# Kernel tuning notes

Hardware: AMD Instinct MI355X
Metric: run time of the kernel (lower is better)

The kernel has to match this reference:

```python
import jax, jax.numpy as jnp
import numpy as np

N_CH = 64
EPS = 1e-5


def _lhat():
    # adj=None branch: dist = ones - eye; adj_dist = exp(-dist/std) (torch.std is unbiased).
    dist = np.ones((N_CH, N_CH), np.float32) - np.eye(N_CH, dtype=np.float32)
    std = dist.std(ddof=1)
    A = np.exp(-dist / std).astype(np.float32)  # all entries > threshold=1e-4 -> fully connected w/ self loops
    deg = A.sum(axis=1)
    dinv = 1.0 / np.sqrt(deg)
    L = np.eye(N_CH, dtype=np.float32) - dinv[:, None] * A * dinv[None, :]  # sym-normalized Laplacian
    # ChebConv rescaling: Lhat = 2L/lambda_max - I with lambda_max=2 -> L - I
    return jnp.asarray(L - np.eye(N_CH, dtype=np.float32))


def _cheb(x, Lhat, W):
    # x: (B, N, Fin), W: (K, Fin, Fout). Chebyshev recursion, bias=False.
    Tx0 = x
    out = jnp.einsum('bnf,fo->bno', Tx0, W[0])
    Tx1 = jnp.einsum('nm,bmf->bnf', Lhat, Tx0)
    out = out + jnp.einsum('bnf,fo->bno', Tx1, W[1])
    for k in range(2, W.shape[0]):
        Tx2 = 2.0 * jnp.einsum('nm,bmf->bnf', Lhat, Tx1) - Tx0
        out = out + jnp.einsum('bnf,fo->bno', Tx2, W[k])
        Tx0, Tx1 = Tx1, Tx2
    return out


def _bn(x, g, b):
    # PyG BatchNorm (training mode): stats over all nodes in the batch -> axes (0,1).
    mu = jnp.mean(x, axis=(0, 1), keepdims=True)
    var = jnp.mean((x - mu) ** 2, axis=(0, 1), keepdims=True)
    return g * (x - mu) * jax.lax.rsqrt(var + EPS) + b


def setup_inputs() -> dict:
    key = jax.random.key(0)
    ks = jax.random.split(key, 4)
    B, F_IN, D = 4096, 256, 128
    x = jax.random.normal(ks[0], (B, N_CH, F_IN), dtype=jnp.float32)
    W1 = jax.random.normal(ks[1], (5, F_IN, D), dtype=jnp.float32) * 0.05
    W2 = jax.random.normal(ks[2], (3, D, D), dtype=jnp.float32) * 0.08
    W3 = jax.random.normal(ks[3], (3, D, D), dtype=jnp.float32) * 0.08
    ones = jnp.ones((D,), jnp.float32)
    zeros = jnp.zeros((D,), jnp.float32)
    return {'x': x, 'W1': W1, 'W2': W2, 'W3': W3,
            'g1': ones, 'b1': zeros, 'g2': ones, 'b2': zeros, 'g3': ones, 'b3': zeros}


def reference(x, W1, W2, W3, g1, b1, g2, b2, g3, b3):
    Lhat = _lhat()
    h = jax.nn.relu(_bn(_cheb(x, Lhat, W1), g1, b1))
    h = jax.nn.relu(_bn(_cheb(h, Lhat, W2), g2, b2))
    h = jax.nn.relu(_bn(_cheb(h, Lhat, W3), g3, b3))
    # global_mean_pool over nodes of each graph (dropout p=0 is identity)
    return jnp.mean(h, axis=1)  # (B, embed_dim)
```

## Files before the change

kernel.cpp:

```cpp
#include <hip/hip_runtime.h>
#include <cmath>


typedef __attribute__((ext_vector_type(8))) short bf16x8;
typedef __attribute__((ext_vector_type(4))) float f32x4;

typedef __attribute__((address_space(1))) const unsigned int guint_t;
typedef __attribute__((address_space(3))) unsigned int luint_t;

constexpr int BATCH = 4096;
constexpr int DCH   = 128;
constexpr float INV_NROWS = 1.0f / 262144.0f;

constexpr size_t OFF_G1   = 0;
constexpr size_t OFF_G2   = 32768;
constexpr size_t OFF_G3   = 49152;
constexpr size_t OFF_SCSH = 65536;
constexpr size_t OFF_PP   = 66304;
constexpr size_t OFF_Y    = 1180416;

struct Coeffs { float a[5]; float b[5]; };

__device__ __forceinline__ unsigned short f2bf(float f) {
  unsigned u = __float_as_uint(f);
  u += 0x7FFFu + ((u >> 16) & 1u);
  return (unsigned short)(u >> 16);
}
__device__ __forceinline__ float bf2f(unsigned short s) {
  return __uint_as_float(((unsigned)s) << 16);
}

__global__ __launch_bounds__(256) void prep_gran(const float* __restrict__ W1,
                                                 const float* __restrict__ W2,
                                                 const float* __restrict__ W3,
                                                 float* __restrict__ ws, Coeffs co)
{
  int id = blockIdx.x * 256 + threadIdx.x;
  const float* W; int CIN, K, r; const float* cf; unsigned short* dst;
  if (id < 8192) {
    W = W1; CIN = 256; K = 5; r = id & 4095;
    cf = (id >= 4096) ? co.b : co.a;
    dst = (unsigned short*)(ws + OFF_G1) + (size_t)id * 8;
  } else if (id < 12288) {
    int e = id - 8192; W = W2; CIN = 128; K = 3; r = e & 2047;
    cf = (e >= 2048) ? co.b : co.a;
    dst = (unsigned short*)(ws + OFF_G2) + (size_t)e * 8;
  } else {
    int e = id - 12288; W = W3; CIN = 128; K = 3; r = e & 2047;
    cf = (e >= 2048) ? co.b : co.a;
    dst = (unsigned short*)(ws + OFF_G3) + (size_t)e * 8;
  }
  int kt  = r >> 9;
  int ct  = (r >> 6) & 7;
  int ln  = r & 63;
  int col = ct * 16 + (ln & 15);
  int f0  = kt * 32 + (ln >> 4) * 8;
  bf16x8 g;
#pragma unroll
  for (int i = 0; i < 8; ++i) {
    float s = 0.f;
    for (int k = 0; k < K; ++k)
      s = fmaf(cf[k], W[((size_t)k * CIN + f0 + i) * DCH + col], s);
    g[i] = (short)f2bf(s);
  }
  *reinterpret_cast<bf16x8*>(dst) = g;
}

template <int CIN, bool FIRST>
__global__ __launch_bounds__(512) void layer_k(
    const float* __restrict__ inF,
    const unsigned short* __restrict__ inB,
    unsigned short* __restrict__ yout,
    const unsigned short* __restrict__ gran,
    const float* __restrict__ scsh,
    float* __restrict__ part)
{
  constexpr int NKT = CIN / 32;
  constexpr int NG  = CIN * 16;

  __shared__ unsigned short sB[CIN * 256];
  __shared__ unsigned short slab[8][1152];
  __shared__ float sJw[4][2][DCH];
  __shared__ float sScale[DCH];
  __shared__ float sShift[DCH];

  const int tid = threadIdx.x;
  const int wv  = tid >> 6;
  const int p   = wv >> 1;
  const int h   = wv & 1;
  const int l   = tid & 63;
  const int lr  = l & 15;
  const int lk  = l >> 4;

  {
    const char* gB = reinterpret_cast<const char*>(gran);
    char* lB = reinterpret_cast<char*>(&sB[0]);
#pragma unroll
    for (int i = 0; i < (CIN * 512) / 8192; ++i) {
      const int c = i * 8 + wv;
      __builtin_amdgcn_global_load_lds(
          (guint_t*)(gB + (size_t)c * 1024 + (size_t)l * 16),
          (luint_t*)(lB + c * 1024), 16, 0, 0);
    }
  }
  if constexpr (!FIRST) {
    if (tid < DCH) {
      sScale[tid] = scsh[tid];
      sShift[tid] = scsh[DCH + tid];
    }
  }
  __syncthreads();

  const bf16x8* sBu = reinterpret_cast<const bf16x8*>(&sB[0]);

  float psum[8], psq[8];
#pragma unroll
  for (int ct = 0; ct < 8; ++ct) { psum[ct] = 0.f; psq[ct] = 0.f; }

#pragma unroll 1
  for (int it = 0; it < 4; ++it) {
    const int batch = blockIdx.x * 16 + it * 4 + p;

    f32x4 acc[8][2];
    f32x4 accJ[8];
#pragma unroll
    for (int ct = 0; ct < 8; ++ct) {
#pragma unroll
      for (int mt = 0; mt < 2; ++mt)
#pragma unroll
        for (int r = 0; r < 4; ++r) acc[ct][mt][r] = 0.f;
#pragma unroll
      for (int r = 0; r < 4; ++r) accJ[ct][r] = 0.f;
    }

#pragma unroll
    for (int kt = 0; kt < NKT; ++kt) {
      bf16x8 af[2];
      float vs[8];
#pragma unroll
      for (int i = 0; i < 8; ++i) vs[i] = 0.f;

      if constexpr (FIRST) {
        const float* ap = inF + ((size_t)batch * 64 + h * 32 + lr) * CIN + kt * 32 + lk * 8;
#pragma unroll
        for (int mt = 0; mt < 2; ++mt) {
          float4 u0 = *reinterpret_cast<const float4*>(ap + (size_t)mt * 16 * CIN);
          float4 u1 = *reinterpret_cast<const float4*>(ap + (size_t)mt * 16 * CIN + 4);
          float v8[8] = {u0.x, u0.y, u0.z, u0.w, u1.x, u1.y, u1.z, u1.w};
#pragma unroll
          for (int i = 0; i < 8; ++i) {
            vs[i] += v8[i];
            af[mt][i] = (short)f2bf(v8[i]);
          }
        }
      } else {
        const int c0 = kt * 32 + lk * 8;
        const float4 s0 = *reinterpret_cast<const float4*>(&sScale[c0]);
        const float4 s1 = *reinterpret_cast<const float4*>(&sScale[c0 + 4]);
        const float4 h0 = *reinterpret_cast<const float4*>(&sShift[c0]);
        const float4 h1 = *reinterpret_cast<const float4*>(&sShift[c0 + 4]);
        const float scv[8] = {s0.x, s0.y, s0.z, s0.w, s1.x, s1.y, s1.z, s1.w};
        const float shv[8] = {h0.x, h0.y, h0.z, h0.w, h1.x, h1.y, h1.z, h1.w};
        const bf16x8* yb = reinterpret_cast<const bf16x8*>(inB + (size_t)batch * 8192);
#pragma unroll
        for (int mt = 0; mt < 2; ++mt) {
          bf16x8 r16 = yb[kt * 256 + (h * 2 + mt) * 64 + l];
#pragma unroll
          for (int i = 0; i < 8; ++i) {
            float hv = fmaxf(fmaf(bf2f((unsigned short)r16[i]), scv[i], shv[i]), 0.f);
            vs[i] += hv;
            af[mt][i] = (short)f2bf(hv);
          }
        }
      }

      bf16x8 asum;
#pragma unroll
      for (int i = 0; i < 8; ++i) asum[i] = (short)f2bf(vs[i]);

      const bf16x8* bI = sBu + kt * 512 + l;
#pragma unroll
      for (int ct = 0; ct < 8; ++ct) {
        bf16x8 fI = bI[ct * 64];
        acc[ct][0] = __builtin_amdgcn_mfma_f32_16x16x32_bf16(af[0], fI, acc[ct][0], 0, 0, 0);
        acc[ct][1] = __builtin_amdgcn_mfma_f32_16x16x32_bf16(af[1], fI, acc[ct][1], 0, 0, 0);
      }
      const bf16x8* bJ = bI + NG;
#pragma unroll
      for (int ct = 0; ct < 8; ++ct)
        accJ[ct] = __builtin_amdgcn_mfma_f32_16x16x32_bf16(asum, bJ[ct * 64], accJ[ct], 0, 0, 0);
    }

#pragma unroll
    for (int ct = 0; ct < 8; ++ct) {
      float t = (accJ[ct][0] + accJ[ct][1]) + (accJ[ct][2] + accJ[ct][3]);
      t += __shfl_xor(t, 16);
      t += __shfl_xor(t, 32);
      if (lk == 0) sJw[p][h][ct * 16 + lr] = t;
    }
    __syncthreads();
    float jv[8];
#pragma unroll
    for (int ct = 0; ct < 8; ++ct)
      jv[ct] = sJw[p][0][ct * 16 + lr] + sJw[p][1][ct * 16 + lr];
    __syncthreads();

    unsigned short* myT = &slab[wv][0];
    bf16x8* yo = reinterpret_cast<bf16x8*>(yout + (size_t)batch * 8192);
#pragma unroll
    for (int mt = 0; mt < 2; ++mt) {
      const int m = h * 2 + mt;
#pragma unroll
      for (int cp = 0; cp < 2; ++cp) {
#pragma unroll
        for (int cq = 0; cq < 4; ++cq) {
          const int ct = cp * 4 + cq;
#pragma unroll
          for (int r = 0; r < 4; ++r) {
            float val = acc[ct][mt][r] + jv[ct];
            psum[ct] += val;
            psq[ct]  = fmaf(val, val, psq[ct]);
            myT[(lk * 4 + r) * 72 + cq * 16 + lr] = f2bf(val);
          }
        }
#pragma unroll
        for (int k2 = 0; k2 < 2; ++k2) {
          bf16x8 gd = *reinterpret_cast<const bf16x8*>(&myT[lr * 72 + k2 * 32 + lk * 8]);
          yo[(cp * 2 + k2) * 256 + m * 64 + l] = gd;
        }
      }
    }
  }

#pragma unroll
  for (int ct = 0; ct < 8; ++ct) {
    psum[ct] += __shfl_xor(psum[ct], 16);
    psum[ct] += __shfl_xor(psum[ct], 32);
    psq[ct]  += __shfl_xor(psq[ct], 16);
    psq[ct]  += __shfl_xor(psq[ct], 32);
  }
  if (lk == 0) {
    float* sRedW = reinterpret_cast<float*>(&slab[wv][0]);
#pragma unroll
    for (int ct = 0; ct < 8; ++ct) {
      sRedW[ct * 16 + lr]       = psum[ct];
      sRedW[128 + ct * 16 + lr] = psq[ct];
    }
  }
  __syncthreads();
  if (tid < 256) {
    const float* base = reinterpret_cast<const float*>(&slab[0][0]);
    float tot = 0.f;
#pragma unroll
    for (int w2 = 0; w2 < 8; ++w2) tot += base[w2 * 576 + tid];
    part[(size_t)blockIdx.x * 256 + tid] = tot;
  }
}

__global__ __launch_bounds__(1024) void finB_k(const float* __restrict__ pp,
                                               const float* __restrict__ gam,
                                               const float* __restrict__ bet,
                                               float* __restrict__ scsh)
{
  __shared__ float red[4][256];
  __shared__ float tot[256];
  const int q = threadIdx.x >> 8, t = threadIdx.x & 255;
  float s = 0.f;
#pragma unroll 8
  for (int i = 0; i < 64; ++i)
    s += pp[(size_t)(q * 64 + i) * 256 + t];
  red[q][t] = s;
  __syncthreads();
  if (q == 0) tot[t] = (red[0][t] + red[1][t]) + (red[2][t] + red[3][t]);
  __syncthreads();
  if (threadIdx.x < 128) {
    float mu  = tot[threadIdx.x] * INV_NROWS;
    float var = tot[128 + threadIdx.x] * INV_NROWS - mu * mu;
    float rs  = rsqrtf(var + 1e-5f);
    float sc  = gam[threadIdx.x] * rs;
    scsh[threadIdx.x]       = sc;
    scsh[128 + threadIdx.x] = fmaf(-mu, sc, bet[threadIdx.x]);
  }
}

__global__ __launch_bounds__(256) void pool_k(const unsigned short* __restrict__ y,
                                              const float* __restrict__ scsh,
                                              float* __restrict__ out)
{
  __shared__ float sYp[64][132];
  __shared__ float sPool[2][DCH];
  const int b = blockIdx.x;
  const int t = threadIdx.x;
  const int wv = t >> 6, l = t & 63;
  const int row = wv * 16 + (l & 15);

#pragma unroll
  for (int kt = 0; kt < 4; ++kt) {
    bf16x8 r16 = *(reinterpret_cast<const bf16x8*>(y + (size_t)b * 8192) + (kt * 256 + t));
    const int feat = kt * 32 + (l >> 4) * 8;
    float4 f0, f1;
    f0.x = bf2f((unsigned short)r16[0]); f0.y = bf2f((unsigned short)r16[1]);
    f0.z = bf2f((unsigned short)r16[2]); f0.w = bf2f((unsigned short)r16[3]);
    f1.x = bf2f((unsigned short)r16[4]); f1.y = bf2f((unsigned short)r16[5]);
    f1.z = bf2f((unsigned short)r16[6]); f1.w = bf2f((unsigned short)r16[7]);
    *reinterpret_cast<float4*>(&sYp[row][feat])     = f0;
    *reinterpret_cast<float4*>(&sYp[row][feat + 4]) = f1;
  }
  __syncthreads();
  {
    const int c = t & 127, rg = t >> 7;
    float sc = scsh[c];
    float sh = scsh[128 + c];
    float s = 0.f;
#pragma unroll 8
    for (int r = rg * 32; r < rg * 32 + 32; ++r)
      s += fmaxf(fmaf(sYp[r][c], sc, sh), 0.f);
    sPool[rg][c] = s;
  }
  __syncthreads();
  if (t < DCH)
    out[(size_t)b * DCH + t] = (sPool[0][t] + sPool[1][t]) * (1.0f / 64.0f);
}

extern "C" void kernel_launch(void* const* d_in, const int* in_sizes, int n_in,
                              void* d_out, int out_size, void* d_ws, size_t ws_size,
                              hipStream_t stream)
{
  const float* x  = (const float*)d_in[0];
  const float* W1 = (const float*)d_in[1];
  const float* W2 = (const float*)d_in[2];
  const float* W3 = (const float*)d_in[3];
  const float* g1 = (const float*)d_in[4];
  const float* b1 = (const float*)d_in[5];
  const float* g2 = (const float*)d_in[6];
  const float* b2 = (const float*)d_in[7];
  const float* g3 = (const float*)d_in[8];
  const float* b3 = (const float*)d_in[9];
  float* out = (float*)d_out;
  float* ws  = (float*)d_ws;

  Coeffs co;
  {
    double sd  = sqrt(63.0 / 4095.0);
    double av  = exp(-1.0 / sd);
    double deg = 1.0 + 63.0 * av;
    double al  = -(1.0 - av) / deg;
    double be  = -av / deg;
    double ak[5], bk[5];
    ak[0] = 1.0; bk[0] = 0.0;
    ak[1] = al;  bk[1] = be;
    for (int k = 2; k < 5; ++k) {
      ak[k] = 2.0 * al * ak[k - 1] - ak[k - 2];
      bk[k] = 2.0 * (be * ak[k - 1] + (al + 64.0 * be) * bk[k - 1]) - bk[k - 2];
    }
    for (int k = 0; k < 5; ++k) { co.a[k] = (float)ak[k]; co.b[k] = (float)bk[k]; }
  }

  const unsigned short* gr1 = (const unsigned short*)(ws + OFF_G1);
  const unsigned short* gr2 = (const unsigned short*)(ws + OFF_G2);
  const unsigned short* gr3 = (const unsigned short*)(ws + OFF_G3);
  float* scsh1 = ws + OFF_SCSH;
  float* scsh2 = scsh1 + 256;
  float* scsh3 = scsh1 + 512;
  float* pp    = ws + OFF_PP;
  unsigned short* yv = (unsigned short*)(ws + OFF_Y);

  prep_gran<<<64, 256, 0, stream>>>(W1, W2, W3, ws, co);

  layer_k<256, true ><<<256, 512, 0, stream>>>(x, nullptr, yv, gr1, nullptr, pp);
  finB_k<<<1, 1024, 0, stream>>>(pp, g1, b1, scsh1);
  layer_k<128, false><<<256, 512, 0, stream>>>(nullptr, yv, yv, gr2, scsh1, pp);
  finB_k<<<1, 1024, 0, stream>>>(pp, g2, b2, scsh2);
  layer_k<128, false><<<256, 512, 0, stream>>>(nullptr, yv, yv, gr3, scsh2, pp);
  finB_k<<<1, 1024, 0, stream>>>(pp, g3, b3, scsh3);
  pool_k<<<BATCH, 256, 0, stream>>>(yv, scsh3, out);

  (void)in_sizes; (void)n_in; (void)out_size; (void)ws_size;
}
```

Baseline: 200.3 us.

## Replace BN finalize kernels with atomic partial sums folded into consumers

```diff
diff --git a/kernel.cpp b/kernel.cpp
--- a/kernel.cpp
+++ b/kernel.cpp
@@ -15,8 +15,7 @@
 constexpr size_t OFF_G1   = 0;
 constexpr size_t OFF_G2   = 32768;
 constexpr size_t OFF_G3   = 49152;
-constexpr size_t OFF_SCSH = 65536;
-constexpr size_t OFF_PP   = 66304;
+constexpr size_t OFF_RAW  = 65536;
 constexpr size_t OFF_Y    = 1180416;
 
 struct Coeffs { float a[5]; float b[5]; };
@@ -33,9 +32,11 @@
 __global__ __launch_bounds__(256) void prep_gran(const float* __restrict__ W1,
                                                  const float* __restrict__ W2,
                                                  const float* __restrict__ W3,
-                                                 float* __restrict__ ws, Coeffs co)
+                                                 float* __restrict__ ws,
+                                                 float* __restrict__ raw, Coeffs co)
 {
   int id = blockIdx.x * 256 + threadIdx.x;
+  if (id < 6144) raw[id] = 0.f;
   const float* W; int CIN, K, r; const float* cf; unsigned short* dst;
   if (id < 8192) {
     W = W1; CIN = 256; K = 5; r = id & 4095;
@@ -72,8 +73,9 @@
     const unsigned short* __restrict__ inB,
     unsigned short* __restrict__ yout,
     const unsigned short* __restrict__ gran,
-    const float* __restrict__ scsh,
-    float* __restrict__ part)
+    const float* __restrict__ rawIn,
+    const float* __restrict__ gam, const float* __restrict__ bet,
+    float* __restrict__ rawOut)
 {
   constexpr int NKT = CIN / 32;
   constexpr int NG  = CIN * 16;
@@ -105,8 +107,18 @@
   }
   if constexpr (!FIRST) {
     if (tid < DCH) {
-      sScale[tid] = scsh[tid];
-      sShift[tid] = scsh[DCH + tid];
+      float ss = 0.f, qq = 0.f;
+#pragma unroll
+      for (int s = 0; s < 8; ++s) {
+        ss += rawIn[s * 256 + tid];
+        qq += rawIn[s * 256 + 128 + tid];
+      }
+      float mu  = ss * INV_NROWS;
+      float var = qq * INV_NROWS - mu * mu;
+      float rs  = rsqrtf(var + 1e-5f);
+      float sc  = gam[tid] * rs;
+      sScale[tid] = sc;
+      sShift[tid] = fmaf(-mu, sc, bet[tid]);
     }
   }
   __syncthreads();
@@ -253,46 +265,39 @@
     float tot = 0.f;
 #pragma unroll
     for (int w2 = 0; w2 < 8; ++w2) tot += base[w2 * 576 + tid];
-    part[(size_t)blockIdx.x * 256 + tid] = tot;
-  }
-}
-
-__global__ __launch_bounds__(1024) void finB_k(const float* __restrict__ pp,
-                                               const float* __restrict__ gam,
-                                               const float* __restrict__ bet,
-                                               float* __restrict__ scsh)
-{
-  __shared__ float red[4][256];
-  __shared__ float tot[256];
-  const int q = threadIdx.x >> 8, t = threadIdx.x & 255;
-  float s = 0.f;
-#pragma unroll 8
-  for (int i = 0; i < 64; ++i)
-    s += pp[(size_t)(q * 64 + i) * 256 + t];
-  red[q][t] = s;
-  __syncthreads();
-  if (q == 0) tot[t] = (red[0][t] + red[1][t]) + (red[2][t] + red[3][t]);
-  __syncthreads();
-  if (threadIdx.x < 128) {
-    float mu  = tot[threadIdx.x] * INV_NROWS;
-    float var = tot[128 + threadIdx.x] * INV_NROWS - mu * mu;
-    float rs  = rsqrtf(var + 1e-5f);
-    float sc  = gam[threadIdx.x] * rs;
-    scsh[threadIdx.x]       = sc;
-    scsh[128 + threadIdx.x] = fmaf(-mu, sc, bet[threadIdx.x]);
+    atomicAdd(&rawOut[(blockIdx.x & 7) * 256 + tid], tot);
   }
 }
 
 __global__ __launch_bounds__(256) void pool_k(const unsigned short* __restrict__ y,
-                                              const float* __restrict__ scsh,
+                                              const float* __restrict__ raw3,
+                                              const float* __restrict__ gam,
+                                              const float* __restrict__ bet,
                                               float* __restrict__ out)
 {
   __shared__ float sYp[64][132];
   __shared__ float sPool[2][DCH];
+  __shared__ float sScale[DCH];
+  __shared__ float sShift[DCH];
   const int b = blockIdx.x;
   const int t = threadIdx.x;
   const int wv = t >> 6, l = t & 63;
   const int row = wv * 16 + (l & 15);
+
+  if (t < DCH) {
+    float ss = 0.f, qq = 0.f;
+#pragma unroll
+    for (int s = 0; s < 8; ++s) {
+      ss += raw3[s * 256 + t];
+      qq += raw3[s * 256 + 128 + t];
+    }
+    float mu  = ss * INV_NROWS;
+    float var = qq * INV_NROWS - mu * mu;
+    float rr  = rsqrtf(var + 1e-5f);
+    float sc  = gam[t] * rr;
+    sScale[t] = sc;
+    sShift[t] = fmaf(-mu, sc, bet[t]);
+  }
 
 #pragma unroll
   for (int kt = 0; kt < 4; ++kt) {
@@ -309,8 +314,8 @@
   __syncthreads();
   {
     const int c = t & 127, rg = t >> 7;
-    float sc = scsh[c];
-    float sh = scsh[128 + c];
+    float sc = sScale[c];
+    float sh = sShift[c];
     float s = 0.f;
 #pragma unroll 8
     for (int r = rg * 32; r < rg * 32 + 32; ++r)
@@ -359,21 +364,20 @@
   const unsigned short* gr1 = (const unsigned short*)(ws + OFF_G1);
   const unsigned short* gr2 = (const unsigned short*)(ws + OFF_G2);
   const unsigned short* gr3 = (const unsigned short*)(ws + OFF_G3);
-  float* scsh1 = ws + OFF_SCSH;
-  float* scsh2 = scsh1 + 256;
-  float* scsh3 = scsh1 + 512;
-  float* pp    = ws + OFF_PP;
+  float* raw1 = ws + OFF_RAW;
+  float* raw2 = raw1 + 2048;
+  float* raw3 = raw1 + 4096;
   unsigned short* yv = (unsigned short*)(ws + OFF_Y);
 
-  prep_gran<<<64, 256, 0, stream>>>(W1, W2, W3, ws, co);
-
-  layer_k<256, true ><<<256, 512, 0, stream>>>(x, nullptr, yv, gr1, nullptr, pp);
-  finB_k<<<1, 1024, 0, stream>>>(pp, g1, b1, scsh1);
-  layer_k<128, false><<<256, 512, 0, stream>>>(nullptr, yv, yv, gr2, scsh1, pp);
-  finB_k<<<1, 1024, 0, stream>>>(pp, g2, b2, scsh2);
-  layer_k<128, false><<<256, 512, 0, stream>>>(nullptr, yv, yv, gr3, scsh2, pp);
-  finB_k<<<1, 1024, 0, stream>>>(pp, g3, b3, scsh3);
-  pool_k<<<BATCH, 256, 0, stream>>>(yv, scsh3, out);
+  prep_gran<<<64, 256, 0, stream>>>(W1, W2, W3, ws, raw1, co);
+
+  layer_k<256, true ><<<256, 512, 0, stream>>>(x, nullptr, yv, gr1,
+                                               nullptr, nullptr, nullptr, raw1);
+  layer_k<128, false><<<256, 512, 0, stream>>>(nullptr, yv, yv, gr2,
+                                               raw1, g1, b1, raw2);
+  layer_k<128, false><<<256, 512, 0, stream>>>(nullptr, yv, yv, gr3,
+                                               raw2, g2, b2, raw3);
+  pool_k<<<BATCH, 256, 0, stream>>>(yv, raw3, g3, b3, out);
 
   (void)in_sizes; (void)n_in; (void)out_size; (void)ws_size;
 }
```

Result: faster. 185.9 us (-7.2%).
